# Kernel tuning notes

Measured on AMD Instinct MI355X. Metric: run time of the kernel, lower is better.

The kernel has to match this reference:

```python
import jax, jax.numpy as jnp
import numpy as np

Ng, Np, B, T = 4096, 512, 128, 100

def setup_inputs() -> dict:
    key = jax.random.key(0)
    ks = jax.random.split(key, 6)
    # xavier-ish scaling for the learned weights
    def xavier(k, shape):
        fan_in, fan_out = shape[1], shape[0]
        lim = jnp.sqrt(6.0 / (fan_in + fan_out))
        return jax.random.uniform(k, shape, jnp.float32, -lim, lim)
    return {
        "v": jax.random.normal(ks[0], (B, T, 2), jnp.float32),
        "p0": jax.random.uniform(ks[1], (B, Np), jnp.float32),
        "W_enc": xavier(ks[2], (Ng, Np)),   # init_position_encoder.weight
        "W_ih": xavier(ks[3], (Ng, 2)),     # RNN weight_ih_l0
        "W_hh": xavier(ks[4], (Ng, Ng)),    # RNN weight_hh_l0
        "W_dec": xavier(ks[5], (Np, Ng)),   # decoder.weight
    }

def reference(v, p0, W_enc, W_ih, W_hh, W_dec):
    # h0 = init_position_encoder(p0): (B, Ng)
    h0 = p0 @ W_enc.T
    # precompute input projections for all steps: (T, B, Ng)
    vin = jnp.einsum('btk,gk->tbg', v, W_ih)

    def step(h, x):
        h_new = jax.nn.relu(x + h @ W_hh.T)  # (B, Ng)
        return h_new, h_new

    _, hs = jax.lax.scan(step, h0, vin)      # hs: (T, B, Ng)
    g = jnp.swapaxes(hs, 0, 1)               # (B, T, Ng)
    preds = g @ W_dec.T                      # (B, T, Np)
    return jax.nn.log_softmax(preds, axis=-1)
```

## Files before the change

kernel.cpp:

```cpp
#include <hip/hip_runtime.h>

#define NG 4096
#define NP 512
#define BSZ 128
#define NT 100

typedef _Float16 f16;
typedef __attribute__((ext_vector_type(8))) _Float16 half8;
typedef __attribute__((ext_vector_type(4))) _Float16 half4v;
typedef __attribute__((ext_vector_type(16))) float f32x16;

__device__ inline f32x16 mfma16(half8 a, half8 b, f32x16 c) {
  return __builtin_amdgcn_mfma_f32_32x32x16_f16(a, b, c, 0, 0, 0);
}
__device__ __forceinline__ void gload16(const void* g, void* l) {
  __builtin_amdgcn_global_load_lds(
      (const __attribute__((address_space(1))) void*)g,
      (__attribute__((address_space(3))) void*)l, 16, 0, 0);
}
__device__ __forceinline__ void pipe_bar8() {
  __builtin_amdgcn_sched_barrier(0);
  asm volatile("s_waitcnt vmcnt(8)" ::: "memory");
  __builtin_amdgcn_s_barrier();
  __builtin_amdgcn_sched_barrier(0);
}
__device__ __forceinline__ void pipe_bar0() {
  __builtin_amdgcn_sched_barrier(0);
  asm volatile("s_waitcnt vmcnt(0)" ::: "memory");
  __builtin_amdgcn_s_barrier();
  __builtin_amdgcn_sched_barrier(0);
}

__global__ __launch_bounds__(256) void conv_all(
    const float* __restrict__ whh, const float* __restrict__ wdec,
    const float* __restrict__ wenc, const float* __restrict__ p0,
    f16* __restrict__ whh16, f16* __restrict__ wdec16,
    f16* __restrict__ wenc16, f16* __restrict__ p016)
{
  int i = blockIdx.x * 256 + threadIdx.x;
  const float* src; f16* dst; int off;
  if (i < 4194304)      { src = whh;  dst = whh16;  off = 0; }
  else if (i < 4718592) { src = wdec; dst = wdec16; off = 4194304; }
  else if (i < 5242880) { src = wenc; dst = wenc16; off = 4718592; }
  else if (i < 5259264) { src = p0;   dst = p016;   off = 5242880; }
  else return;
  const int j = i - off;
  const float4 x = ((const float4*)src)[j];
  half4v h = { (f16)x.x, (f16)x.y, (f16)x.z, (f16)x.w };
  *(half4v*)&dst[(size_t)j * 4] = h;
}

template<int NS, int KROW>
__global__ __launch_bounds__(256, 1) void gemm_ksplit(
    const f16* __restrict__ bmat, const f16* __restrict__ amat,
    f16* __restrict__ part)
{
  constexpr int NCH = KROW / (NS * 64);
  __shared__ __align__(128) char lds[3 * 32768];
  const int tid = threadIdx.x;
  const int w = tid >> 6, lane = tid & 63;
  const int wm = w & 1, wn = w >> 1;
  const int l31 = lane & 31, hi = lane >> 5;
  const int n0 = blockIdx.y * 128;
  const int k0 = blockIdx.x * (KROW / NS);
  constexpr size_t krb = (size_t)KROW * 2;

  const int lrow8 = lane >> 3;
  const int swz = ((lane & 7) ^ lrow8) * 16;
  const char* gA = (const char*)amat;
  const char* gB = (const char*)bmat + (size_t)n0 * krb;

  f32x16 acc[2][2] = {};

  auto stage = [&](int buf, int c) {
    const size_t kb = (size_t)((k0 + c * 64) * 2) + swz;
    char* lb = lds + buf * 32768;
    #pragma unroll
    for (int j = 0; j < 4; ++j) {
      const int r = w * 32 + j * 8;
      gload16(gA + (size_t)(r + lrow8) * krb + kb, lb + r * 128);
      gload16(gB + (size_t)(r + lrow8) * krb + kb, lb + 16384 + r * 128);
    }
  };
  auto compute = [&](int buf) {
    const char* bA = lds + buf * 32768;
    const char* bB = bA + 16384;
    const int swr = (lane & 7) << 4;
    #pragma unroll
    for (int kk = 0; kk < 4; ++kk) {
      const int bc = (kk * 32 + (hi << 4)) ^ swr;
      half8 a0 = *(const half8*)(bA + (wm * 64 + l31) * 128 + bc);
      half8 a1 = *(const half8*)(bA + (wm * 64 + 32 + l31) * 128 + bc);
      half8 b0 = *(const half8*)(bB + (wn * 64 + l31) * 128 + bc);
      half8 b1 = *(const half8*)(bB + (wn * 64 + 32 + l31) * 128 + bc);
      acc[0][0] = mfma16(a0, b0, acc[0][0]);
      acc[0][1] = mfma16(a0, b1, acc[0][1]);
      acc[1][0] = mfma16(a1, b0, acc[1][0]);
      acc[1][1] = mfma16(a1, b1, acc[1][1]);
    }
  };

  stage(0, 0);
  stage(1, 1);
  pipe_bar8();
  #pragma unroll 1
  for (int c = 0; c < NCH - 2; ++c) {
    stage((c + 2) % 3, c + 2);
    compute(c % 3);
    pipe_bar8();
  }
  compute((NCH - 2) % 3);
  pipe_bar0();
  compute((NCH - 1) % 3);

  f16* po = part + (size_t)blockIdx.x * (BSZ * NG);
  #pragma unroll
  for (int mf = 0; mf < 2; ++mf) {
    #pragma unroll
    for (int q = 0; q < 16; ++q) {
      const int row = wm * 64 + mf * 32 + (q & 3) + 8 * (q >> 2) + 4 * hi;
      #pragma unroll
      for (int nf = 0; nf < 2; ++nf) {
        const int col = n0 + wn * 64 + nf * 32 + l31;
        po[(size_t)row * NG + col] = (f16)acc[mf][nf][q];
      }
    }
  }
}

template<int NS, int DOBIAS>
__global__ __launch_bounds__(256) void reduce_kernel(
    const f16* __restrict__ part, const float* __restrict__ v,
    const float* __restrict__ wih, f16* __restrict__ hout, int t)
{
  const int i = blockIdx.x * 256 + threadIdx.x;
  const int b = i >> 10;
  const int gi = (i & 1023) * 4;
  const half4v* p = (const half4v*)part + (((size_t)b * NG + gi) >> 2);
  float s[4];
  half4v q0 = p[0];
  #pragma unroll
  for (int j = 0; j < 4; ++j) s[j] = (float)q0[j];
  #pragma unroll
  for (int k = 1; k < NS; ++k) {
    half4v q = p[(size_t)k * (BSZ * NG / 4)];
    #pragma unroll
    for (int j = 0; j < 4; ++j) s[j] += (float)q[j];
  }
  half4v h;
  if (DOBIAS) {
    const float2 vb = *(const float2*)&v[((size_t)b * NT + t) * 2];
    const float4 wA = *(const float4*)(wih + (size_t)gi * 2);
    const float4 wB = *(const float4*)(wih + (size_t)gi * 2 + 4);
    h[0] = (f16)fmaxf(s[0] + vb.x * wA.x + vb.y * wA.y, 0.f);
    h[1] = (f16)fmaxf(s[1] + vb.x * wA.z + vb.y * wA.w, 0.f);
    h[2] = (f16)fmaxf(s[2] + vb.x * wB.x + vb.y * wB.y, 0.f);
    h[3] = (f16)fmaxf(s[3] + vb.x * wB.z + vb.y * wB.w, 0.f);
  } else {
    #pragma unroll
    for (int j = 0; j < 4; ++j) h[j] = (f16)s[j];
  }
  *(half4v*)&hout[(size_t)b * NG + gi] = h;
}

__global__ __launch_bounds__(512, 2) void decode_kernel(
    const f16* __restrict__ hs, const f16* __restrict__ wdec16,
    float* __restrict__ out)
{
  __shared__ __align__(128) char lds[2 * 73728];
  __shared__ float redm[8][64];
  __shared__ float reds[8][64];
  __shared__ float gLS[64];
  const int tid = threadIdx.x;
  const int w = tid >> 6, lane = tid & 63;
  const int l31 = lane & 31, hi = lane >> 5;
  const int r0 = blockIdx.x * 64;

  const int lrow8 = lane >> 3;
  const int swz = ((lane & 7) ^ lrow8) * 16;
  const char* gA = (const char*)(hs + (size_t)r0 * NG);
  const char* gB = (const char*)wdec16;

  f32x16 acc[2][2] = {};

  auto stage = [&](int buf, int c) {
    const size_t kb = (size_t)(c * 128) + swz;
    char* lb = lds + buf * 73728;
    gload16(gA + (size_t)(w * 8 + lrow8) * (NG * 2) + kb, lb + w * 1024);
    #pragma unroll
    for (int j = 0; j < 8; ++j) {
      const int r = w * 64 + j * 8;
      gload16(gB + (size_t)(r + lrow8) * (NG * 2) + kb, lb + 8192 + r * 128);
    }
  };
  auto compute = [&](int buf) {
    const char* bA = lds + buf * 73728;
    const char* bB = bA + 8192;
    const int swr = (lane & 7) << 4;
    #pragma unroll
    for (int kk = 0; kk < 4; ++kk) {
      const int bc = (kk * 32 + (hi << 4)) ^ swr;
      half8 a0 = *(const half8*)(bA + l31 * 128 + bc);
      half8 a1 = *(const half8*)(bA + (32 + l31) * 128 + bc);
      half8 b0 = *(const half8*)(bB + (w * 64 + l31) * 128 + bc);
      half8 b1 = *(const half8*)(bB + (w * 64 + 32 + l31) * 128 + bc);
      acc[0][0] = mfma16(a0, b0, acc[0][0]);
      acc[0][1] = mfma16(a0, b1, acc[0][1]);
      acc[1][0] = mfma16(a1, b0, acc[1][0]);
      acc[1][1] = mfma16(a1, b1, acc[1][1]);
    }
  };

  stage(0, 0);
  __syncthreads();
  #pragma unroll 1
  for (int c = 0; c < 64; ++c) {
    if (c < 63) stage((c + 1) & 1, c + 1);
    compute(c & 1);
    __syncthreads();
  }

  #pragma unroll
  for (int mf = 0; mf < 2; ++mf) {
    #pragma unroll
    for (int q = 0; q < 16; ++q) {
      float m = fmaxf(acc[mf][0][q], acc[mf][1][q]);
      #pragma unroll
      for (int d = 1; d < 32; d <<= 1) m = fmaxf(m, __shfl_xor(m, d));
      if (l31 == q) redm[w][mf * 32 + (q & 3) + 8 * (q >> 2) + 4 * hi] = m;
    }
  }
  __syncthreads();
  if (tid < 64) {
    float M = redm[0][tid];
    #pragma unroll
    for (int ww = 1; ww < 8; ++ww) M = fmaxf(M, redm[ww][tid]);
    gLS[tid] = M;
  }
  __syncthreads();
  #pragma unroll
  for (int mf = 0; mf < 2; ++mf) {
    #pragma unroll
    for (int q = 0; q < 16; ++q) {
      const int rl = mf * 32 + (q & 3) + 8 * (q >> 2) + 4 * hi;
      const float M = gLS[rl];
      float e = __expf(acc[mf][0][q] - M) + __expf(acc[mf][1][q] - M);
      #pragma unroll
      for (int d = 1; d < 32; d <<= 1) e += __shfl_xor(e, d);
      if (l31 == q) reds[w][rl] = e;
    }
  }
  __syncthreads();
  if (tid < 64) {
    float S = reds[0][tid];
    #pragma unroll
    for (int ww = 1; ww < 8; ++ww) S += reds[ww][tid];
    gLS[tid] = gLS[tid] + __logf(S);
  }
  __syncthreads();
  #pragma unroll
  for (int mf = 0; mf < 2; ++mf) {
    #pragma unroll
    for (int q = 0; q < 16; ++q) {
      const int rl = mf * 32 + (q & 3) + 8 * (q >> 2) + 4 * hi;
      const int r = r0 + rl;
      const int tt = r >> 7, b = r & 127;
      const float lg = gLS[rl];
      float* orow = out + ((size_t)b * NT + tt) * NP + w * 64 + l31;
      orow[0]  = acc[mf][0][q] - lg;
      orow[32] = acc[mf][1][q] - lg;
    }
  }
}


extern "C" void kernel_launch(void* const* d_in, const int* in_sizes, int n_in,
                              void* d_out, int out_size, void* d_ws, size_t ws_size,
                              hipStream_t stream)
{
  const float* v    = (const float*)d_in[0];
  const float* p0   = (const float*)d_in[1];
  const float* wenc = (const float*)d_in[2];
  const float* wih  = (const float*)d_in[3];
  const float* whh  = (const float*)d_in[4];
  const float* wdec = (const float*)d_in[5];
  float* out = (float*)d_out;
  char* ws = (char*)d_ws;

  f16* whh16  = (f16*)(ws);
  f16* wdec16 = (f16*)(ws + 33554432);
  f16* wenc16 = (f16*)(ws + 37748736);
  f16* p016   = (f16*)(ws + 41943040);
  f16* h016   = (f16*)(ws + 42074112);
  f16* hs     = (f16*)(ws + 43122688);
  f16* part   = (f16*)d_out;
  const size_t BNG = (size_t)BSZ * NG;

  conv_all<<<dim3(20544), dim3(256), 0, stream>>>(
      whh, wdec, wenc, p0, whh16, wdec16, wenc16, p016);

  gemm_ksplit<2, 512><<<dim3(2, 32), dim3(256), 0, stream>>>(wenc16, p016, part);
  reduce_kernel<2, 0><<<dim3(512), dim3(256), 0, stream>>>(part, v, wih, h016, 0);

  for (int t = 0; t < NT; ++t) {
    const f16* hp = (t == 0) ? h016 : hs + (size_t)(t - 1) * BNG;
    gemm_ksplit<8, 4096><<<dim3(8, 32), dim3(256), 0, stream>>>(whh16, hp, part);
    reduce_kernel<8, 1><<<dim3(512), dim3(256), 0, stream>>>(part, v, wih, hs + (size_t)t * BNG, t);
  }
  decode_kernel<<<dim3(200), dim3(512), 0, stream>>>(hs, wdec16, out);
}
```

Measured before the change: 1.350 ms.

## Triple-buffer decode GEMM with smaller K chunks and vmcnt-based barriers

The decode GEMM's staging moves from a double-buffered 128-byte K chunk with full __syncthreads to a three-buffer ring of 64-byte K chunks. Partial `s_waitcnt vmcnt(4)` barriers let the next two chunks' global-to-LDS loads stay in flight while the current chunk is computed. The LDS swizzle is reworked for the narrower rows, and launch bounds drop to one block per CU. The goal is to hide load latency and shrink LDS use, at the cost of twice as many barrier steps and fewer MFMAs per sync.

```diff
diff --git a/kernel.cpp b/kernel.cpp
--- a/kernel.cpp
+++ b/kernel.cpp
@@ -21,6 +21,12 @@
 __device__ __forceinline__ void pipe_bar8() {
   __builtin_amdgcn_sched_barrier(0);
   asm volatile("s_waitcnt vmcnt(8)" ::: "memory");
+  __builtin_amdgcn_s_barrier();
+  __builtin_amdgcn_sched_barrier(0);
+}
+__device__ __forceinline__ void pipe_bar4() {
+  __builtin_amdgcn_sched_barrier(0);
+  asm volatile("s_waitcnt vmcnt(4)" ::: "memory");
   __builtin_amdgcn_s_barrier();
   __builtin_amdgcn_sched_barrier(0);
 }
@@ -163,11 +169,12 @@
   *(half4v*)&hout[(size_t)b * NG + gi] = h;
 }
 
-__global__ __launch_bounds__(512, 2) void decode_kernel(
+__global__ __launch_bounds__(512, 1) void decode_kernel(
     const f16* __restrict__ hs, const f16* __restrict__ wdec16,
     float* __restrict__ out)
 {
-  __shared__ __align__(128) char lds[2 * 73728];
+  constexpr int NCH = 128;
+  __shared__ __align__(128) char lds[3 * 36864];
   __shared__ float redm[8][64];
   __shared__ float reds[8][64];
   __shared__ float gLS[64];
@@ -176,34 +183,38 @@
   const int l31 = lane & 31, hi = lane >> 5;
   const int r0 = blockIdx.x * 64;
 
-  const int lrow8 = lane >> 3;
-  const int swz = ((lane & 7) ^ lrow8) * 16;
   const char* gA = (const char*)(hs + (size_t)r0 * NG);
   const char* gB = (const char*)wdec16;
 
   f32x16 acc[2][2] = {};
 
   auto stage = [&](int buf, int c) {
-    const size_t kb = (size_t)(c * 128) + swz;
-    char* lb = lds + buf * 73728;
-    gload16(gA + (size_t)(w * 8 + lrow8) * (NG * 2) + kb, lb + w * 1024);
-    #pragma unroll
-    for (int j = 0; j < 8; ++j) {
-      const int r = w * 64 + j * 8;
-      gload16(gB + (size_t)(r + lrow8) * (NG * 2) + kb, lb + 8192 + r * 128);
+    char* lb = lds + buf * 36864;
+    const size_t kb = (size_t)c * 64;
+    if (w < 4) {
+      const int row = w * 16 + (lane >> 2);
+      const int u = (lane & 3) ^ ((row >> 1) & 3);
+      gload16(gA + (size_t)row * (NG * 2) + kb + u * 16, lb + w * 1024 + lane * 16);
+    }
+    #pragma unroll
+    for (int j = 0; j < 4; ++j) {
+      const int row = (w * 4 + j) * 16 + (lane >> 2);
+      const int u = (lane & 3) ^ ((row >> 1) & 3);
+      gload16(gB + (size_t)row * (NG * 2) + kb + u * 16,
+              lb + 4096 + (w * 4 + j) * 1024 + lane * 16);
     }
   };
   auto compute = [&](int buf) {
-    const char* bA = lds + buf * 73728;
-    const char* bB = bA + 8192;
-    const int swr = (lane & 7) << 4;
-    #pragma unroll
-    for (int kk = 0; kk < 4; ++kk) {
-      const int bc = (kk * 32 + (hi << 4)) ^ swr;
-      half8 a0 = *(const half8*)(bA + l31 * 128 + bc);
-      half8 a1 = *(const half8*)(bA + (32 + l31) * 128 + bc);
-      half8 b0 = *(const half8*)(bB + (w * 64 + l31) * 128 + bc);
-      half8 b1 = *(const half8*)(bB + (w * 64 + 32 + l31) * 128 + bc);
+    const char* bA = lds + buf * 36864;
+    const char* bB = bA + 4096;
+    const int sw = (l31 >> 1) & 3;
+    #pragma unroll
+    for (int kk = 0; kk < 2; ++kk) {
+      const int ub = ((kk * 2 + hi) ^ sw) * 16;
+      half8 a0 = *(const half8*)(bA + l31 * 64 + ub);
+      half8 a1 = *(const half8*)(bA + (l31 + 32) * 64 + ub);
+      half8 b0 = *(const half8*)(bB + (w * 64 + l31) * 64 + ub);
+      half8 b1 = *(const half8*)(bB + (w * 64 + 32 + l31) * 64 + ub);
       acc[0][0] = mfma16(a0, b0, acc[0][0]);
       acc[0][1] = mfma16(a0, b1, acc[0][1]);
       acc[1][0] = mfma16(a1, b0, acc[1][0]);
@@ -212,13 +223,17 @@
   };
 
   stage(0, 0);
-  __syncthreads();
+  stage(1, 1);
+  pipe_bar4();
   #pragma unroll 1
-  for (int c = 0; c < 64; ++c) {
-    if (c < 63) stage((c + 1) & 1, c + 1);
-    compute(c & 1);
-    __syncthreads();
-  }
+  for (int c = 0; c < NCH - 2; ++c) {
+    stage((c + 2) % 3, c + 2);
+    compute(c % 3);
+    pipe_bar4();
+  }
+  compute((NCH - 2) % 3);
+  pipe_bar0();
+  compute((NCH - 1) % 3);
 
   #pragma unroll
   for (int mf = 0; mf < 2; ++mf) {
```

Result: no change. 1.375 ms (+1.9%).
